# Optimization experiments

Hardware: AMD Instinct MI355X
Metric: run time of the kernel (lower is better)

## Reference

```python
import jax, jax.numpy as jnp
import numpy as np

EMB_DIM = 256
NUM_EMB = 1024
COMMITMENT = 0.25
DECAY = 0.9
EPS = 1e-5
B, H, W = 32, 64, 64


def setup_inputs() -> dict:
    key = jax.random.key(0)
    k1, k2 = jax.random.split(key)
    x = jax.random.normal(k1, (B, EMB_DIM, H, W), dtype=jnp.float32)
    embed = jax.random.normal(k2, (EMB_DIM, NUM_EMB), dtype=jnp.float32)
    cluster_size = jnp.zeros((NUM_EMB,), dtype=jnp.float32)
    ema_embed = embed  # registered as embed.clone() in the torch module
    return {"x": x, "embed": embed, "cluster_size": cluster_size, "ema_embed": ema_embed}


def reference(x, embed, cluster_size, ema_embed):
    # x: [B, C, H, W] -> [B, H, W, C]
    xp = jnp.transpose(x, (0, 2, 3, 1))
    flat = xp.reshape(-1, EMB_DIM)  # [N, D]
    # squared-distance matrix [N, K]
    dist = (jnp.sum(flat * flat, axis=1, keepdims=True)
            - 2.0 * (flat @ embed)
            + jnp.sum(embed * embed, axis=0, keepdims=True))
    embed_idx_flat = jnp.argmin(dist, axis=1)  # [N]
    embed_idx = embed_idx_flat.reshape(xp.shape[:-1])  # [B, H, W]
    quantize = embed.T[embed_idx]  # gather -> [B, H, W, D]

    # training-mode EMA codebook update (buffer updates in torch)
    ref_count = jax.ops.segment_sum(jnp.ones_like(embed_idx_flat, dtype=flat.dtype),
                                    embed_idx_flat, num_segments=NUM_EMB)  # [K]
    new_cluster_size = cluster_size * DECAY + (1.0 - DECAY) * ref_count
    n = jnp.sum(new_cluster_size)
    smoothing = n * ((new_cluster_size + EPS) / (n + new_cluster_size * EPS))
    # dw = flatten^T @ onehot, computed as a segment sum: [K, D] -> [D, K]
    dw = jax.ops.segment_sum(flat, embed_idx_flat, num_segments=NUM_EMB).T
    new_ema_embed = ema_embed * DECAY + (1.0 - DECAY) * dw
    new_embed = new_ema_embed / smoothing[None, :]

    e_latent_loss = jnp.mean((jax.lax.stop_gradient(quantize) - xp) ** 2)
    loss = COMMITMENT * e_latent_loss
    # straight-through estimator
    quantize_st = xp + jax.lax.stop_gradient(quantize - xp)
    out = jnp.transpose(quantize_st, (0, 3, 1, 2))  # [B, C, H, W]
    return out, loss, embed_idx, new_embed, new_cluster_size, new_ema_embed
```

## Files before the change

kernel.cpp:

```cpp
#include <hip/hip_runtime.h>
#include <cfloat>
#include <cstdint>

typedef unsigned short u16;

#define NTOK   131072
#define DIM    256
#define NCODE  1024
#define HW     4096
#define PLANE  1048576
#define DECAYF 0.9f
#define EPSF   1e-5f

#define O_OUT     0
#define O_LOSS    33554432
#define O_IDX     33554433
#define O_NEWEMB  33685505
#define O_NCS     33947649
#define O_NEE     33948673

#define P_XS      0
#define P_V1      16777216
#define P_V2      17825792
#define P_KK      18874368
#define P_VF      19922944
#define P_DW      20054016
#define P_BT      22151168
#define P_ENORM64 22413312

#define WS_ENORM  0
#define WS_CNT    1024
#define WS_LOSS   2048
#define WS_RC     2049
#define WS_LIST   2050
#define WS_SMOOTH 34818

#define REF_CAP 32768
#define DELTA   0.25f
#define RT      16

typedef __attribute__((ext_vector_type(8))) short bf16x8;
typedef __attribute__((ext_vector_type(4))) float f32x4;

__device__ __forceinline__ u16 bf16_rne(float f) {
    unsigned int u = __float_as_uint(f);
    unsigned int r = u + 0x7FFF + ((u >> 16) & 1);
    return (u16)(r >> 16);
}
__device__ __forceinline__ float bf16_to_f(u16 s) {
    return __uint_as_float(((unsigned int)s) << 16);
}
__device__ __forceinline__ void gload_lds16(const void* g, void* l) {
    __builtin_amdgcn_global_load_lds(
        (const __attribute__((address_space(1))) unsigned int*)g,
        (__attribute__((address_space(3))) unsigned int*)l, 16, 0, 0);
}

__global__ void k_enorm(const float* __restrict__ embed, float* __restrict__ enorm,
                        double* __restrict__ enorm64) {
    int k = blockIdx.x * 256 + threadIdx.x;
    double s = 0.0;
    for (int d = 0; d < DIM; ++d) {
        float e = embed[(size_t)d * NCODE + k];
        s += (double)e * (double)e;
    }
    enorm[k] = (float)s;
    enorm64[k] = s;
}

__global__ __launch_bounds__(256) void k_xs(const float* __restrict__ x,
                                            u16* __restrict__ Xs,
                                            float* __restrict__ loss_acc)
{
    __shared__ float tile[64 * 65];
    __shared__ float red[256];
    const int tid = threadIdx.x;
    const int blk = blockIdx.x;
    const int b = blk >> 8;
    const int dc = (blk >> 6) & 3;
    const int hwc = blk & 63;
    const int d0 = dc * 64, hw0 = hwc * 64;
    const int r = tid >> 2, s = tid & 3;
    float sq = 0.f;
#pragma unroll
    for (int j = 0; j < 4; ++j) {
        float4 v = *(const float4*)&x[(size_t)b * PLANE + (size_t)(d0 + r) * HW + hw0 + s * 16 + j * 4];
        int c = s * 16 + j * 4;
        tile[r * 65 + c + 0] = v.x; tile[r * 65 + c + 1] = v.y;
        tile[r * 65 + c + 2] = v.z; tile[r * 65 + c + 3] = v.w;
        sq = fmaf(v.x, v.x, sq); sq = fmaf(v.y, v.y, sq);
        sq = fmaf(v.z, v.z, sq); sq = fmaf(v.w, v.w, sq);
    }
    __syncthreads();
    const int tk = tid >> 2, dq = tid & 3;
    u16 us[16];
#pragma unroll
    for (int j = 0; j < 16; ++j)
        us[j] = bf16_rne(tile[(dq * 16 + j) * 65 + tk]);
    size_t ob = (size_t)(b * 4096 + hw0 + tk) * 256 + d0 + dq * 16;
    *(uint4*)&Xs[ob]     = *(uint4*)&us[0];
    *(uint4*)&Xs[ob + 8] = *(uint4*)&us[8];
    red[tid] = sq; __syncthreads();
    for (int st = 128; st > 0; st >>= 1) {
        if (tid < st) red[tid] += red[tid + st];
        __syncthreads();
    }
    if (tid == 0) atomicAdd(loss_acc, red[0]);
}

__global__ __launch_bounds__(256) void k_bt(const float* __restrict__ embed, u16* __restrict__ Bt)
{
    const int tile = blockIdx.x;
    const int cc = tile >> 4, kc = tile & 15;
    const int seg = kc >> 3, dbase = (kc & 7) * 32;
    const int tid = threadIdx.x;
#pragma unroll
    for (int g2 = 0; g2 < 2; ++g2) {
        int p = g2 * 256 + tid;
        int n = p >> 2, s = p & 3, lg = (s - n) & 3;
        int code = cc * 128 + n;
        u16 us[8];
#pragma unroll
        for (int e = 0; e < 8; ++e) {
            int d = dbase + lg * 8 + e;
            float E = embed[(size_t)d * NCODE + code];
            u16 hi = bf16_rne(E);
            us[e] = seg ? bf16_rne(E - bf16_to_f(hi)) : hi;
        }
        *(uint4*)&Bt[(size_t)tile * 4096 + (size_t)p * 8] = *(uint4*)&us[0];
    }
}

__global__ __launch_bounds__(256) void k_dist(
    const u16* __restrict__ Xs, const u16* __restrict__ Bt,
    const float* __restrict__ enorm,
    float* __restrict__ pv1, float* __restrict__ pv2, float* __restrict__ pkk)
{
    __shared__ __align__(16) u16 lds[12288];
    const int tid = threadIdx.x;
    const int w = tid >> 6, l = tid & 63;
    const int cc = blockIdx.x >> 10;
    const int n0 = (blockIdx.x & 1023) * 128;
    const int mh = w & 1, nh = w >> 1;
    const int lane15 = l & 15, quad = l >> 4;

    const u16* src[6];
    u16* dst[6];
#pragma unroll
    for (int r = 0; r < 6; ++r) {
        int p = r * 256 + w * 64 + l;
        dst[r] = &lds[(size_t)(r * 256 + w * 64) * 8];
        if (p < 512) {
            int m = p >> 2, s = p & 3, lg = (s - m) & 3;
            src[r] = Xs + (size_t)(n0 + m) * 256 + lg * 8;
        } else {
            int q = p - 512;
            int kcb = (q >> 9) * 8;
            int qq = q & 511;
            src[r] = Bt + (size_t)(cc * 16 + kcb) * 4096 + (size_t)qq * 8;
        }
    }

    f32x4 acc[4][4];
#pragma unroll
    for (int i = 0; i < 4; ++i)
#pragma unroll
        for (int j = 0; j < 4; ++j) acc[i][j] = (f32x4)0.f;

    for (int kc8 = 0; kc8 < 8; ++kc8) {
        __syncthreads();
#pragma unroll
        for (int r = 0; r < 6; ++r) {
            const u16* s = src[r] + (r < 2 ? (size_t)kc8 * 32 : (size_t)kc8 * 4096);
            gload_lds16(s, dst[r]);
        }
        __syncthreads();

        bf16x8 af[4];
#pragma unroll
        for (int mt = 0; mt < 4; ++mt) {
            int m = mh * 64 + mt * 16 + lane15;
            int slot = (quad + m) & 3;
            af[mt] = *(const bf16x8*)&lds[(size_t)(m * 4 + slot) * 8];
        }
#pragma unroll
        for (int seg = 0; seg < 2; ++seg) {
#pragma unroll
            for (int nt = 0; nt < 4; ++nt) {
                int n = nh * 64 + nt * 16 + lane15;
                int slot = (quad + n) & 3;
                bf16x8 bfr = *(const bf16x8*)&lds[(size_t)(512 + seg * 512 + n * 4 + slot) * 8];
#pragma unroll
                for (int mt = 0; mt < 4; ++mt)
                    acc[mt][nt] = __builtin_amdgcn_mfma_f32_16x16x32_bf16(af[mt], bfr, acc[mt][nt], 0, 0, 0);
            }
        }
    }

    float ev[4]; int ec[4];
#pragma unroll
    for (int nt = 0; nt < 4; ++nt) {
        ec[nt] = cc * 128 + nh * 64 + nt * 16 + lane15;
        ev[nt] = enorm[ec[nt]];
    }
    float r1[4][4], r2[4][4]; int rk[4][4];
#pragma unroll
    for (int mt = 0; mt < 4; ++mt)
#pragma unroll
        for (int rg = 0; rg < 4; ++rg) {
            float v1 = FLT_MAX, v2 = FLT_MAX; int k1 = 1 << 30;
#pragma unroll
            for (int nt = 0; nt < 4; ++nt) {
                float d = fmaf(-2.f, acc[mt][nt][rg], ev[nt]);
                if (d < v1) { v2 = v1; v1 = d; k1 = ec[nt]; }
                else v2 = fminf(v2, d);
            }
            r1[mt][rg] = v1; r2[mt][rg] = v2; rk[mt][rg] = k1;
        }
#pragma unroll
    for (int mask = 1; mask <= 8; mask <<= 1) {
#pragma unroll
        for (int mt = 0; mt < 4; ++mt)
#pragma unroll
            for (int rg = 0; rg < 4; ++rg) {
                float ov1 = __shfl_xor(r1[mt][rg], mask);
                float ov2 = __shfl_xor(r2[mt][rg], mask);
                int   ok  = __shfl_xor(rk[mt][rg], mask);
                if (ov1 < r1[mt][rg] || (ov1 == r1[mt][rg] && ok < rk[mt][rg])) {
                    r2[mt][rg] = fminf(r1[mt][rg], ov2);
                    r1[mt][rg] = ov1; rk[mt][rg] = ok;
                } else {
                    r2[mt][rg] = fminf(r2[mt][rg], ov1);
                }
            }
    }
    __syncthreads();
    float* epi = (float*)lds;
    if (lane15 == 0) {
#pragma unroll
        for (int mt = 0; mt < 4; ++mt)
#pragma unroll
            for (int rg = 0; rg < 4; ++rg) {
                int t = mh * 64 + mt * 16 + quad * 4 + rg;
                float* p = &epi[(nh * 128 + t) * 3];
                p[0] = r1[mt][rg]; p[1] = r2[mt][rg]; p[2] = __int_as_float(rk[mt][rg]);
            }
    }
    __syncthreads();
    if (tid < 128) {
        const float* p0 = &epi[tid * 3];
        const float* p1 = &epi[(128 + tid) * 3];
        float v1 = p0[0], v2 = p0[1]; int k1 = __float_as_int(p0[2]);
        float a1 = p1[0], a2 = p1[1]; int ak = __float_as_int(p1[2]);
        if (a1 < v1 || (a1 == v1 && ak < k1)) { v2 = fminf(v1, a2); v1 = a1; k1 = ak; }
        else v2 = fminf(v2, a1);
        size_t o = (size_t)cc * NTOK + n0 + tid;
        pv1[o] = v1; pv2[o] = v2; pkk[o] = (float)k1;
    }
}

__global__ __launch_bounds__(256) void k_amin(
    const float* __restrict__ pv1, const float* __restrict__ pv2, const float* __restrict__ pkk,
    float* __restrict__ out_idx, float* __restrict__ vf, float* __restrict__ loss_acc,
    int* __restrict__ refcnt, int* __restrict__ reflist)
{
    const int n = blockIdx.x * 256 + threadIdx.x;
    float v1 = FLT_MAX, v2 = FLT_MAX; int k1 = 1 << 30;
    for (int cc = 0; cc < 8; ++cc) {
        float a1 = pv1[(size_t)cc * NTOK + n], a2 = pv2[(size_t)cc * NTOK + n];
        int ak = (int)pkk[(size_t)cc * NTOK + n];
        if (a1 < v1 || (a1 == v1 && ak < k1)) { v2 = fminf(v1, a2); v1 = a1; k1 = ak; }
        else v2 = fminf(v2, a1);
    }
    out_idx[n] = (float)k1;
    vf[n] = v1;
    if (v2 - v1 < DELTA) {
        int pos = atomicAdd(refcnt, 1);
        if (pos < REF_CAP) reflist[pos] = n;
    }
    __shared__ float red[256];
    red[threadIdx.x] = v1; __syncthreads();
    for (int s = 128; s > 0; s >>= 1) {
        if (threadIdx.x < s) red[threadIdx.x] += red[threadIdx.x + s];
        __syncthreads();
    }
    if (threadIdx.x == 0) atomicAdd(loss_acc, red[0]);
}

__global__ __launch_bounds__(256) void k_refine(
    const float* __restrict__ x, const float* __restrict__ embed,
    const double* __restrict__ enorm64,
    float* __restrict__ out_idx, const int* __restrict__ refcnt,
    const int* __restrict__ reflist, const float* __restrict__ vf,
    float* __restrict__ loss_acc)
{
    __shared__ double xm2[RT][DIM];
    __shared__ int toks[RT];
    __shared__ double wv[4][RT];
    __shared__ int wk[4][RT];
    const int tid = threadIdx.x;
    const int w = tid >> 6, l = tid & 63;
    const int cnt = min(*refcnt, REF_CAP);
    for (int base = blockIdx.x * RT; base < cnt; base += gridDim.x * RT) {
        const int nb = min(RT, cnt - base);
        for (int j = 0; j < nb; ++j) {
            int n = reflist[base + j];
            if (tid == 0) toks[j] = n;
            int b = n >> 12, hw = n & 4095;
            float xv = x[(size_t)b * PLANE + (size_t)tid * HW + hw];
            xm2[j][tid] = -2.0 * (double)xv;
        }
        __syncthreads();

        double bv[RT]; int bk[RT];
#pragma unroll
        for (int j = 0; j < RT; ++j) { bv[j] = 1e300; bk[j] = 0; }
#pragma unroll 1
        for (int c = 0; c < 4; ++c) {
            const int k = c * 256 + tid;
            double acc[RT];
#pragma unroll
            for (int j = 0; j < RT; ++j) acc[j] = 0.0;
            const float* ep = embed + k;
#pragma unroll 4
            for (int d = 0; d < DIM; ++d) {
                double ed = (double)ep[(size_t)d * NCODE];
#pragma unroll
                for (int j = 0; j < RT; ++j)
                    acc[j] = fma(ed, xm2[j][d], acc[j]);
            }
            double e2 = enorm64[k];
#pragma unroll
            for (int j = 0; j < RT; ++j) {
                double dist = e2 + acc[j];
                if (dist < bv[j]) { bv[j] = dist; bk[j] = k; }
            }
        }

#pragma unroll
        for (int j = 0; j < RT; ++j) {
            double v = bv[j]; int kk = bk[j];
#pragma unroll
            for (int m = 1; m < 64; m <<= 1) {
                double ov = __shfl_xor(v, m);
                int ok = __shfl_xor(kk, m);
                if (ov < v || (ov == v && ok < kk)) { v = ov; kk = ok; }
            }
            if (l == 0) { wv[w][j] = v; wk[w][j] = kk; }
        }
        __syncthreads();
        if (tid < nb) {
            double v = wv[0][tid]; int kk = wk[0][tid];
#pragma unroll
            for (int wi = 1; wi < 4; ++wi) {
                double ov = wv[wi][tid]; int ok = wk[wi][tid];
                if (ov < v || (ov == v && ok < kk)) { v = ov; kk = ok; }
            }
            int n = toks[tid];
            out_idx[n] = (float)kk;
            atomicAdd(loss_acc, (float)(v - (double)vf[n]));
        }
        __syncthreads();
    }
}

__global__ __launch_bounds__(256) void k_cnt(const float* __restrict__ out_idx, float* __restrict__ cnt) {
    const int n = blockIdx.x * 256 + threadIdx.x;
    atomicAdd(&cnt[(int)out_idx[n]], 1.0f);
}

__global__ __launch_bounds__(256) void k_dw(
    const float* __restrict__ x, const float* __restrict__ out_idx, float* __restrict__ part)
{
    __shared__ float tile[NCODE * 9];
    const int tid = threadIdx.x;
    const int slice = blockIdx.x & 31;
    const int chunk = blockIdx.x >> 5;
    const int d0 = slice * 8;
    for (int i = tid; i < NCODE * 9; i += 256) tile[i] = 0.f;
    __syncthreads();
    const int nbeg = chunk * (NTOK / 8);
    for (int t = tid; t < NTOK / 8; t += 256) {
        const int n = nbeg + t;
        const int b = n >> 12, hw = n & 4095;
        const int k = (int)out_idx[n];
        const float* xb = x + (size_t)b * PLANE + hw;
        float* tp = tile + k * 9;
#pragma unroll
        for (int dl = 0; dl < 8; ++dl)
            unsafeAtomicAdd(&tp[dl], xb[(size_t)(d0 + dl) * HW]);
    }
    __syncthreads();
    for (int i = tid; i < 8 * NCODE; i += 256) {
        const int dl = i >> 10, k = i & (NCODE - 1);
        part[((size_t)chunk * DIM + d0 + dl) * NCODE + k] = tile[k * 9 + dl];
    }
}

__global__ __launch_bounds__(1024) void k_fin_cs(
    const float* __restrict__ cs_in, const float* __restrict__ cnt,
    float* __restrict__ out_ncs, float* __restrict__ smooth)
{
    const int k = threadIdx.x;
    float ncs = cs_in[k] * DECAYF + (1.f - DECAYF) * cnt[k];
    out_ncs[k] = ncs;
    __shared__ float red[1024];
    red[k] = ncs; __syncthreads();
    for (int s = 512; s > 0; s >>= 1) {
        if (k < s) red[k] += red[k + s];
        __syncthreads();
    }
    float n = red[0];
    smooth[k] = n * ((ncs + EPSF) / (n + ncs * EPSF));
}

__global__ __launch_bounds__(256) void k_fin_emb(
    const float* __restrict__ ema, const float* __restrict__ part,
    const float* __restrict__ smooth, float* __restrict__ out_ne, float* __restrict__ out_nee)
{
    const int i = blockIdx.x * 256 + threadIdx.x;
    const int k = i & (NCODE - 1);
    float dw = 0.f;
    for (int c = 0; c < 8; ++c) dw += part[(size_t)c * (DIM * NCODE) + i];
    float nee = ema[i] * DECAYF + (1.f - DECAYF) * dw;
    out_nee[i] = nee;
    out_ne[i] = nee / smooth[k];
}

__global__ __launch_bounds__(256) void k_quant(
    const float* __restrict__ embed, const float* __restrict__ out_idx, float* __restrict__ out_q)
{
    const int n = blockIdx.x * 256 + threadIdx.x;
    const int b = n >> 12, hw = n & 4095;
    const int idx = (int)out_idx[n];
    const size_t base = (size_t)b * PLANE + hw;
    for (int d = 0; d < DIM; ++d)
        out_q[base + (size_t)d * HW] = embed[(size_t)d * NCODE + idx];
}

__global__ void k_loss(const float* __restrict__ loss_acc, float* __restrict__ out_loss) {
    out_loss[0] = 0.25f * loss_acc[0] / 33554432.f;
}

extern "C" void kernel_launch(void* const* d_in, const int* in_sizes, int n_in,
                              void* d_out, int out_size, void* d_ws, size_t ws_size,
                              hipStream_t stream) {
    const float* x     = (const float*)d_in[0];
    const float* embed = (const float*)d_in[1];
    const float* csz   = (const float*)d_in[2];
    const float* ema   = (const float*)d_in[3];
    float* out = (float*)d_out;
    float* ws  = (float*)d_ws;

    u16* Xs = (u16*)(out + P_XS);
    u16* Bt = (u16*)(out + P_BT);
    double* enorm64 = (double*)(out + P_ENORM64);

    hipMemsetAsync(ws + WS_CNT, 0, (size_t)(WS_RC + 1 - WS_CNT) * sizeof(float), stream);

    k_enorm<<<4, 256, 0, stream>>>(embed, ws + WS_ENORM, enorm64);
    k_xs<<<8192, 256, 0, stream>>>(x, Xs, ws + WS_LOSS);
    k_bt<<<128, 256, 0, stream>>>(embed, Bt);
    k_dist<<<8192, 256, 0, stream>>>(Xs, Bt, ws + WS_ENORM,
                                     out + P_V1, out + P_V2, out + P_KK);
    k_amin<<<NTOK / 256, 256, 0, stream>>>(out + P_V1, out + P_V2, out + P_KK,
                                           out + O_IDX, out + P_VF, ws + WS_LOSS,
                                           (int*)(ws + WS_RC), (int*)(ws + WS_LIST));
    k_refine<<<1024, 256, 0, stream>>>(x, embed, enorm64, out + O_IDX,
                                       (const int*)(ws + WS_RC), (const int*)(ws + WS_LIST),
                                       out + P_VF, ws + WS_LOSS);
    k_cnt<<<NTOK / 256, 256, 0, stream>>>(out + O_IDX, ws + WS_CNT);
    k_dw<<<256, 256, 0, stream>>>(x, out + O_IDX, out + P_DW);
    k_fin_cs<<<1, 1024, 0, stream>>>(csz, ws + WS_CNT, out + O_NCS, ws + WS_SMOOTH);
    k_fin_emb<<<1024, 256, 0, stream>>>(ema, out + P_DW, ws + WS_SMOOTH,
                                        out + O_NEWEMB, out + O_NEE);
    k_quant<<<NTOK / 256, 256, 0, stream>>>(embed, out + O_IDX, out + O_OUT);
    k_loss<<<1, 1, 0, stream>>>(ws + WS_LOSS, out + O_LOSS);
}
```

Measured before the change: 1.215 ms.

## Fuse argmin into distance GEMM with resident X tile and triple-buffered codebook

Each distance block now owns 128 tokens and loops over all 8 code chunks. The full X tile stays resident in LDS, and codebook slices stream through a 3-deep ring with explicit vmcnt waits. The running top-2 reduction is done in registers, which removes the partial-result buffers and the separate k_amin kernel. The LDS swizzle also changes (an extra m>>2 term) to reduce bank conflicts. In exchange it uses about 119KB of LDS per block, which limits occupancy to one block per CU, and the grid drops to 1024 blocks.

```diff
diff --git a/kernel.cpp b/kernel.cpp
--- a/kernel.cpp
+++ b/kernel.cpp
@@ -20,9 +20,6 @@
 #define O_NEE     33948673
 
 #define P_XS      0
-#define P_V1      16777216
-#define P_V2      17825792
-#define P_KK      18874368
 #define P_VF      19922944
 #define P_DW      20054016
 #define P_BT      22151168
@@ -117,7 +114,7 @@
 #pragma unroll
     for (int g2 = 0; g2 < 2; ++g2) {
         int p = g2 * 256 + tid;
-        int n = p >> 2, s = p & 3, lg = (s - n) & 3;
+        int n = p >> 2, s = p & 3, lg = (s - n - (n >> 2)) & 3;
         int code = cc * 128 + n;
         u16 us[8];
 #pragma unroll
@@ -134,157 +131,166 @@
 __global__ __launch_bounds__(256) void k_dist(
     const u16* __restrict__ Xs, const u16* __restrict__ Bt,
     const float* __restrict__ enorm,
-    float* __restrict__ pv1, float* __restrict__ pv2, float* __restrict__ pkk)
-{
-    __shared__ __align__(16) u16 lds[12288];
+    float* __restrict__ out_idx, float* __restrict__ vfo, float* __restrict__ loss_acc,
+    int* __restrict__ refcnt, int* __restrict__ reflist)
+{
+    __shared__ __align__(16) u16 lds[60928];
     const int tid = threadIdx.x;
     const int w = tid >> 6, l = tid & 63;
-    const int cc = blockIdx.x >> 10;
-    const int n0 = (blockIdx.x & 1023) * 128;
+    const int n0 = blockIdx.x * 128;
     const int mh = w & 1, nh = w >> 1;
     const int lane15 = l & 15, quad = l >> 4;
 
-    const u16* src[6];
-    u16* dst[6];
-#pragma unroll
-    for (int r = 0; r < 6; ++r) {
-        int p = r * 256 + w * 64 + l;
-        dst[r] = &lds[(size_t)(r * 256 + w * 64) * 8];
-        if (p < 512) {
-            int m = p >> 2, s = p & 3, lg = (s - m) & 3;
-            src[r] = Xs + (size_t)(n0 + m) * 256 + lg * 8;
-        } else {
-            int q = p - 512;
-            int kcb = (q >> 9) * 8;
-            int qq = q & 511;
-            src[r] = Bt + (size_t)(cc * 16 + kcb) * 4096 + (size_t)qq * 8;
-        }
-    }
-
-    f32x4 acc[4][4];
-#pragma unroll
-    for (int i = 0; i < 4; ++i)
-#pragma unroll
-        for (int j = 0; j < 4; ++j) acc[i][j] = (f32x4)0.f;
-
-    for (int kc8 = 0; kc8 < 8; ++kc8) {
-        __syncthreads();
-#pragma unroll
-        for (int r = 0; r < 6; ++r) {
-            const u16* s = src[r] + (r < 2 ? (size_t)kc8 * 32 : (size_t)kc8 * 4096);
-            gload_lds16(s, dst[r]);
-        }
-        __syncthreads();
-
-        bf16x8 af[4];
-#pragma unroll
-        for (int mt = 0; mt < 4; ++mt) {
-            int m = mh * 64 + mt * 16 + lane15;
-            int slot = (quad + m) & 3;
-            af[mt] = *(const bf16x8*)&lds[(size_t)(m * 4 + slot) * 8];
-        }
-#pragma unroll
-        for (int seg = 0; seg < 2; ++seg) {
-#pragma unroll
-            for (int nt = 0; nt < 4; ++nt) {
-                int n = nh * 64 + nt * 16 + lane15;
-                int slot = (quad + n) & 3;
-                bf16x8 bfr = *(const bf16x8*)&lds[(size_t)(512 + seg * 512 + n * 4 + slot) * 8];
-#pragma unroll
-                for (int mt = 0; mt < 4; ++mt)
-                    acc[mt][nt] = __builtin_amdgcn_mfma_f32_16x16x32_bf16(af[mt], bfr, acc[mt][nt], 0, 0, 0);
-            }
-        }
-    }
-
-    float ev[4]; int ec[4];
-#pragma unroll
-    for (int nt = 0; nt < 4; ++nt) {
-        ec[nt] = cc * 128 + nh * 64 + nt * 16 + lane15;
-        ev[nt] = enorm[ec[nt]];
-    }
-    float r1[4][4], r2[4][4]; int rk[4][4];
-#pragma unroll
-    for (int mt = 0; mt < 4; ++mt)
-#pragma unroll
-        for (int rg = 0; rg < 4; ++rg) {
-            float v1 = FLT_MAX, v2 = FLT_MAX; int k1 = 1 << 30;
-#pragma unroll
-            for (int nt = 0; nt < 4; ++nt) {
-                float d = fmaf(-2.f, acc[mt][nt][rg], ev[nt]);
-                if (d < v1) { v2 = v1; v1 = d; k1 = ec[nt]; }
-                else v2 = fminf(v2, d);
-            }
-            r1[mt][rg] = v1; r2[mt][rg] = v2; rk[mt][rg] = k1;
-        }
-#pragma unroll
-    for (int mask = 1; mask <= 8; mask <<= 1) {
+#pragma unroll
+    for (int rr = 0; rr < 16; ++rr) {
+        int p = rr * 256 + tid;
+        int kc8p = p >> 9;
+        int q = p & 511;
+        int m = q >> 2, s = q & 3;
+        int lg = (s - m - (m >> 2)) & 3;
+        gload_lds16(Xs + (size_t)(n0 + m) * 256 + kc8p * 32 + lg * 8,
+                    &lds[(size_t)(rr * 256 + w * 64) * 8]);
+    }
+    gload_lds16((const char*)enorm + (size_t)tid * 16,
+                &lds[58880 + (size_t)(w * 64) * 8]);
+
+#define STAGE_B(cc_, kc8_, ring_) do {                                               \
+    _Pragma("unroll")                                                                \
+    for (int rr_ = 0; rr_ < 4; ++rr_) {                                              \
+        int p_ = rr_ * 256 + tid;                                                    \
+        int seg_ = p_ >> 9;                                                          \
+        gload_lds16(Bt + (size_t)((cc_) * 16 + seg_ * 8 + (kc8_)) * 4096             \
+                       + (size_t)(p_ & 511) * 8,                                     \
+                    &lds[32768 + (ring_) * 8192 + (size_t)(rr_ * 256 + w * 64) * 8]); \
+    } } while (0)
+
+    STAGE_B(0, 0, 0);
+    STAGE_B(0, 1, 1);
+
+    float rv1 = FLT_MAX, rv2 = FLT_MAX; int rk1 = 1 << 30;
+    float* epi = (float*)&lds[57344];
+    const float* enf = (const float*)&lds[58880];
+
+    for (int cc = 0; cc < 8; ++cc) {
+        f32x4 acc[4][4];
+#pragma unroll
+        for (int i = 0; i < 4; ++i)
+#pragma unroll
+            for (int j = 0; j < 4; ++j) acc[i][j] = (f32x4)0.f;
+
+#pragma unroll
+        for (int kc8 = 0; kc8 < 8; ++kc8) {
+            const int i = cc * 8 + kc8;
+            if (cc == 7 && kc8 == 7) asm volatile("s_waitcnt vmcnt(0)" ::: "memory");
+            else                     asm volatile("s_waitcnt vmcnt(4)" ::: "memory");
+            __builtin_amdgcn_s_barrier();
+
+            if (i + 2 < 64) {
+                const int i2 = i + 2;
+                STAGE_B(i2 >> 3, i2 & 7, i2 % 3);
+            }
+
+            const u16* bufB = &lds[32768 + (i % 3) * 8192];
+            bf16x8 af[4];
+#pragma unroll
+            for (int mt = 0; mt < 4; ++mt) {
+                int m = mh * 64 + mt * 16 + lane15;
+                int slot = (quad + m + (m >> 2)) & 3;
+                af[mt] = *(const bf16x8*)&lds[(size_t)kc8 * 4096 + (size_t)(m * 4 + slot) * 8];
+            }
+#pragma unroll
+            for (int seg = 0; seg < 2; ++seg)
+#pragma unroll
+                for (int nt = 0; nt < 4; ++nt) {
+                    int n = nh * 64 + nt * 16 + lane15;
+                    int slot = (quad + n + (n >> 2)) & 3;
+                    bf16x8 bfr = *(const bf16x8*)&bufB[(size_t)(seg * 512 + n * 4 + slot) * 8];
+#pragma unroll
+                    for (int mt = 0; mt < 4; ++mt)
+                        acc[mt][nt] = __builtin_amdgcn_mfma_f32_16x16x32_bf16(af[mt], bfr, acc[mt][nt], 0, 0, 0);
+                }
+        }
+
+        float ev[4]; int ec[4];
+#pragma unroll
+        for (int nt = 0; nt < 4; ++nt) {
+            ec[nt] = cc * 128 + nh * 64 + nt * 16 + lane15;
+            ev[nt] = enf[ec[nt]];
+        }
+        float r1[4][4], r2[4][4]; int rk[4][4];
 #pragma unroll
         for (int mt = 0; mt < 4; ++mt)
 #pragma unroll
             for (int rg = 0; rg < 4; ++rg) {
-                float ov1 = __shfl_xor(r1[mt][rg], mask);
-                float ov2 = __shfl_xor(r2[mt][rg], mask);
-                int   ok  = __shfl_xor(rk[mt][rg], mask);
-                if (ov1 < r1[mt][rg] || (ov1 == r1[mt][rg] && ok < rk[mt][rg])) {
-                    r2[mt][rg] = fminf(r1[mt][rg], ov2);
-                    r1[mt][rg] = ov1; rk[mt][rg] = ok;
-                } else {
-                    r2[mt][rg] = fminf(r2[mt][rg], ov1);
+                float v1 = FLT_MAX, v2 = FLT_MAX; int k1 = 1 << 30;
+#pragma unroll
+                for (int nt = 0; nt < 4; ++nt) {
+                    float d = fmaf(-2.f, acc[mt][nt][rg], ev[nt]);
+                    if (d < v1) { v2 = v1; v1 = d; k1 = ec[nt]; }
+                    else v2 = fminf(v2, d);
                 }
-            }
+                r1[mt][rg] = v1; r2[mt][rg] = v2; rk[mt][rg] = k1;
+            }
+#pragma unroll
+        for (int mask = 1; mask <= 8; mask <<= 1) {
+#pragma unroll
+            for (int mt = 0; mt < 4; ++mt)
+#pragma unroll
+                for (int rg = 0; rg < 4; ++rg) {
+                    float ov1 = __shfl_xor(r1[mt][rg], mask);
+                    float ov2 = __shfl_xor(r2[mt][rg], mask);
+                    int   ok  = __shfl_xor(rk[mt][rg], mask);
+                    if (ov1 < r1[mt][rg] || (ov1 == r1[mt][rg] && ok < rk[mt][rg])) {
+                        r2[mt][rg] = fminf(r1[mt][rg], ov2);
+                        r1[mt][rg] = ov1; rk[mt][rg] = ok;
+                    } else {
+                        r2[mt][rg] = fminf(r2[mt][rg], ov1);
+                    }
+                }
+        }
+        if (lane15 == 0) {
+#pragma unroll
+            for (int mt = 0; mt < 4; ++mt)
+#pragma unroll
+                for (int rg = 0; rg < 4; ++rg) {
+                    int t = mh * 64 + mt * 16 + quad * 4 + rg;
+                    float* p = &epi[(nh * 128 + t) * 3];
+                    p[0] = r1[mt][rg]; p[1] = r2[mt][rg]; p[2] = __int_as_float(rk[mt][rg]);
+                }
+        }
+        asm volatile("s_waitcnt lgkmcnt(0)" ::: "memory");
+        __builtin_amdgcn_s_barrier();
+        if (tid < 128) {
+            const float* p0 = &epi[tid * 3];
+            const float* p1 = &epi[(128 + tid) * 3];
+            float v1 = p0[0], v2 = p0[1]; int k1 = __float_as_int(p0[2]);
+            float a1 = p1[0], a2 = p1[1]; int ak = __float_as_int(p1[2]);
+            if (a1 < v1 || (a1 == v1 && ak < k1)) { v2 = fminf(v1, a2); v1 = a1; k1 = ak; }
+            else v2 = fminf(v2, a1);
+            if (v1 < rv1 || (v1 == rv1 && k1 < rk1)) { rv2 = fminf(rv1, v2); rv1 = v1; rk1 = k1; }
+            else rv2 = fminf(rv2, v1);
+        }
+    }
+
+    if (tid < 128) {
+        int n = n0 + tid;
+        out_idx[n] = (float)rk1;
+        vfo[n] = rv1;
+        if (rv2 - rv1 < DELTA) {
+            int pos = atomicAdd(refcnt, 1);
+            if (pos < REF_CAP) reflist[pos] = n;
+        }
     }
     __syncthreads();
-    float* epi = (float*)lds;
-    if (lane15 == 0) {
-#pragma unroll
-        for (int mt = 0; mt < 4; ++mt)
-#pragma unroll
-            for (int rg = 0; rg < 4; ++rg) {
-                int t = mh * 64 + mt * 16 + quad * 4 + rg;
-                float* p = &epi[(nh * 128 + t) * 3];
-                p[0] = r1[mt][rg]; p[1] = r2[mt][rg]; p[2] = __int_as_float(rk[mt][rg]);
-            }
-    }
+    float* red = epi;
+    red[tid] = (tid < 128) ? rv1 : 0.f;
     __syncthreads();
-    if (tid < 128) {
-        const float* p0 = &epi[tid * 3];
-        const float* p1 = &epi[(128 + tid) * 3];
-        float v1 = p0[0], v2 = p0[1]; int k1 = __float_as_int(p0[2]);
-        float a1 = p1[0], a2 = p1[1]; int ak = __float_as_int(p1[2]);
-        if (a1 < v1 || (a1 == v1 && ak < k1)) { v2 = fminf(v1, a2); v1 = a1; k1 = ak; }
-        else v2 = fminf(v2, a1);
-        size_t o = (size_t)cc * NTOK + n0 + tid;
-        pv1[o] = v1; pv2[o] = v2; pkk[o] = (float)k1;
-    }
-}
-
-__global__ __launch_bounds__(256) void k_amin(
-    const float* __restrict__ pv1, const float* __restrict__ pv2, const float* __restrict__ pkk,
-    float* __restrict__ out_idx, float* __restrict__ vf, float* __restrict__ loss_acc,
-    int* __restrict__ refcnt, int* __restrict__ reflist)
-{
-    const int n = blockIdx.x * 256 + threadIdx.x;
-    float v1 = FLT_MAX, v2 = FLT_MAX; int k1 = 1 << 30;
-    for (int cc = 0; cc < 8; ++cc) {
-        float a1 = pv1[(size_t)cc * NTOK + n], a2 = pv2[(size_t)cc * NTOK + n];
-        int ak = (int)pkk[(size_t)cc * NTOK + n];
-        if (a1 < v1 || (a1 == v1 && ak < k1)) { v2 = fminf(v1, a2); v1 = a1; k1 = ak; }
-        else v2 = fminf(v2, a1);
-    }
-    out_idx[n] = (float)k1;
-    vf[n] = v1;
-    if (v2 - v1 < DELTA) {
-        int pos = atomicAdd(refcnt, 1);
-        if (pos < REF_CAP) reflist[pos] = n;
-    }
-    __shared__ float red[256];
-    red[threadIdx.x] = v1; __syncthreads();
     for (int s = 128; s > 0; s >>= 1) {
-        if (threadIdx.x < s) red[threadIdx.x] += red[threadIdx.x + s];
-        __syncthreads();
-    }
-    if (threadIdx.x == 0) atomicAdd(loss_acc, red[0]);
+        if (tid < s) red[tid] += red[tid + s];
+        __syncthreads();
+    }
+    if (tid == 0) atomicAdd(loss_acc, red[0]);
+#undef STAGE_B
 }
 
 __global__ __launch_bounds__(256) void k_refine(
@@ -461,11 +467,9 @@
     k_enorm<<<4, 256, 0, stream>>>(embed, ws + WS_ENORM, enorm64);
     k_xs<<<8192, 256, 0, stream>>>(x, Xs, ws + WS_LOSS);
     k_bt<<<128, 256, 0, stream>>>(embed, Bt);
-    k_dist<<<8192, 256, 0, stream>>>(Xs, Bt, ws + WS_ENORM,
-                                     out + P_V1, out + P_V2, out + P_KK);
-    k_amin<<<NTOK / 256, 256, 0, stream>>>(out + P_V1, out + P_V2, out + P_KK,
-                                           out + O_IDX, out + P_VF, ws + WS_LOSS,
-                                           (int*)(ws + WS_RC), (int*)(ws + WS_LIST));
+    k_dist<<<1024, 256, 0, stream>>>(Xs, Bt, ws + WS_ENORM,
+                                     out + O_IDX, out + P_VF, ws + WS_LOSS,
+                                     (int*)(ws + WS_RC), (int*)(ws + WS_LIST));
     k_refine<<<1024, 256, 0, stream>>>(x, embed, enorm64, out + O_IDX,
                                        (const int*)(ws + WS_RC), (const int*)(ws + WS_LIST),
                                        out + P_VF, ws + WS_LOSS);
```

After: 1.303 ms. 1.07x slower.

## Add fp32 refinement pass before fp64 refine, routing only near-ties to double

Applied to the files above, without the earlier changes.

Inserts an fp32 re-scoring kernel for tokens flagged by the bf16 distance pass. Tokens whose top-2 fp32 gap exceeds a margin are finalised there. Only the remaining near-ties go to a hard list that the existing fp64 refine kernel processes. This cuts the expensive double-precision work on MI355X, at the risk that the fp32 margin occasionally picks a different argmin than fp64 would.

```diff
diff --git a/kernel.cpp b/kernel.cpp
--- a/kernel.cpp
+++ b/kernel.cpp
@@ -27,16 +27,19 @@
 #define P_DW      20054016
 #define P_BT      22151168
 #define P_ENORM64 22413312
+#define P_HLIST   22415360
 
 #define WS_ENORM  0
 #define WS_CNT    1024
 #define WS_LOSS   2048
 #define WS_RC     2049
-#define WS_LIST   2050
-#define WS_SMOOTH 34818
+#define WS_RC2    2050
+#define WS_LIST   2051
+#define WS_SMOOTH 34819
 
 #define REF_CAP 32768
 #define DELTA   0.25f
+#define MARGIN  0.03f
 #define RT      16
 
 typedef __attribute__((ext_vector_type(8))) short bf16x8;
@@ -287,11 +290,107 @@
     if (threadIdx.x == 0) atomicAdd(loss_acc, red[0]);
 }
 
-__global__ __launch_bounds__(256) void k_refine(
+__global__ __launch_bounds__(256) void k_ref32(
+    const float* __restrict__ x, const float* __restrict__ embed,
+    const float* __restrict__ enorm,
+    float* __restrict__ out_idx, const int* __restrict__ refcnt,
+    const int* __restrict__ reflist, const float* __restrict__ vf,
+    float* __restrict__ loss_acc, int* __restrict__ hardcnt, int* __restrict__ hardlist)
+{
+    __shared__ float xm2t[DIM][RT + 1];
+    __shared__ int toks[RT];
+    __shared__ float wv1[4][RT], wv2[4][RT];
+    __shared__ int wk1[4][RT];
+    const int tid = threadIdx.x;
+    const int w = tid >> 6;
+    const int cnt = min(*refcnt, REF_CAP);
+    for (int base = blockIdx.x * RT; base < cnt; base += gridDim.x * RT) {
+        const int nb = min(RT, cnt - base);
+        for (int j = 0; j < nb; ++j) {
+            int n = reflist[base + j];
+            if (tid == 0) toks[j] = n;
+            int b = n >> 12, hw = n & 4095;
+            xm2t[tid][j] = -2.f * x[(size_t)b * PLANE + (size_t)tid * HW + hw];
+        }
+        if (nb < RT)
+            for (int j = nb; j < RT; ++j) xm2t[tid][j] = 0.f;
+        __syncthreads();
+
+        float b1[RT], b2[RT]; int k1[RT];
+#pragma unroll
+        for (int j = 0; j < RT; ++j) { b1[j] = FLT_MAX; b2[j] = FLT_MAX; k1[j] = 1 << 30; }
+#pragma unroll 1
+        for (int c = 0; c < 4; ++c) {
+            const int k = c * 256 + tid;
+            float acc[RT];
+#pragma unroll
+            for (int j = 0; j < RT; ++j) acc[j] = 0.f;
+#pragma unroll 1
+            for (int d0 = 0; d0 < DIM; d0 += 8) {
+                float er[8];
+#pragma unroll
+                for (int dd = 0; dd < 8; ++dd)
+                    er[dd] = embed[(size_t)(d0 + dd) * NCODE + k];
+#pragma unroll
+                for (int dd = 0; dd < 8; ++dd)
+#pragma unroll
+                    for (int j = 0; j < RT; ++j)
+                        acc[j] = fmaf(er[dd], xm2t[d0 + dd][j], acc[j]);
+            }
+            float e2 = enorm[k];
+#pragma unroll
+            for (int j = 0; j < RT; ++j) {
+                float dist = e2 + acc[j];
+                if (dist < b1[j]) { b2[j] = b1[j]; b1[j] = dist; k1[j] = k; }
+                else b2[j] = fminf(b2[j], dist);
+            }
+        }
+
+#pragma unroll
+        for (int m = 1; m < 64; m <<= 1) {
+#pragma unroll
+            for (int j = 0; j < RT; ++j) {
+                float ov1 = __shfl_xor(b1[j], m);
+                float ov2 = __shfl_xor(b2[j], m);
+                int   ok  = __shfl_xor(k1[j], m);
+                if (ov1 < b1[j] || (ov1 == b1[j] && ok < k1[j])) {
+                    b2[j] = fminf(b1[j], ov2); b1[j] = ov1; k1[j] = ok;
+                } else {
+                    b2[j] = fminf(b2[j], ov1);
+                }
+            }
+        }
+        if ((tid & 63) == 0) {
+#pragma unroll
+            for (int j = 0; j < RT; ++j) { wv1[w][j] = b1[j]; wk1[w][j] = k1[j]; wv2[w][j] = b2[j]; }
+        }
+        __syncthreads();
+        if (tid < nb) {
+            float v1 = wv1[0][tid], v2 = wv2[0][tid]; int kk = wk1[0][tid];
+#pragma unroll
+            for (int wi = 1; wi < 4; ++wi) {
+                float a1 = wv1[wi][tid], a2 = wv2[wi][tid]; int ak = wk1[wi][tid];
+                if (a1 < v1 || (a1 == v1 && ak < kk)) { v2 = fminf(v1, a2); v1 = a1; kk = ak; }
+                else v2 = fminf(v2, a1);
+            }
+            int n = toks[tid];
+            if (v2 - v1 > MARGIN) {
+                out_idx[n] = (float)kk;
+                atomicAdd(loss_acc, v1 - vf[n]);
+            } else {
+                int pos = atomicAdd(hardcnt, 1);
+                hardlist[pos] = n;
+            }
+        }
+        __syncthreads();
+    }
+}
+
+__global__ __launch_bounds__(256) void k_ref64(
     const float* __restrict__ x, const float* __restrict__ embed,
     const double* __restrict__ enorm64,
-    float* __restrict__ out_idx, const int* __restrict__ refcnt,
-    const int* __restrict__ reflist, const float* __restrict__ vf,
+    float* __restrict__ out_idx, const int* __restrict__ hcnt,
+    const int* __restrict__ hlist, const float* __restrict__ vf,
     float* __restrict__ loss_acc)
 {
     __shared__ double xm2[RT][DIM];
@@ -300,11 +399,11 @@
     __shared__ int wk[4][RT];
     const int tid = threadIdx.x;
     const int w = tid >> 6, l = tid & 63;
-    const int cnt = min(*refcnt, REF_CAP);
+    const int cnt = min(*hcnt, REF_CAP);
     for (int base = blockIdx.x * RT; base < cnt; base += gridDim.x * RT) {
         const int nb = min(RT, cnt - base);
         for (int j = 0; j < nb; ++j) {
-            int n = reflist[base + j];
+            int n = hlist[base + j];
             if (tid == 0) toks[j] = n;
             int b = n >> 12, hw = n & 4095;
             float xv = x[(size_t)b * PLANE + (size_t)tid * HW + hw];
@@ -456,7 +555,7 @@
     u16* Bt = (u16*)(out + P_BT);
     double* enorm64 = (double*)(out + P_ENORM64);
 
-    hipMemsetAsync(ws + WS_CNT, 0, (size_t)(WS_RC + 1 - WS_CNT) * sizeof(float), stream);
+    hipMemsetAsync(ws + WS_CNT, 0, (size_t)(WS_RC2 + 1 - WS_CNT) * sizeof(float), stream);
 
     k_enorm<<<4, 256, 0, stream>>>(embed, ws + WS_ENORM, enorm64);
     k_xs<<<8192, 256, 0, stream>>>(x, Xs, ws + WS_LOSS);
@@ -466,9 +565,13 @@
     k_amin<<<NTOK / 256, 256, 0, stream>>>(out + P_V1, out + P_V2, out + P_KK,
                                            out + O_IDX, out + P_VF, ws + WS_LOSS,
                                            (int*)(ws + WS_RC), (int*)(ws + WS_LIST));
-    k_refine<<<1024, 256, 0, stream>>>(x, embed, enorm64, out + O_IDX,
-                                       (const int*)(ws + WS_RC), (const int*)(ws + WS_LIST),
-                                       out + P_VF, ws + WS_LOSS);
+    k_ref32<<<2048, 256, 0, stream>>>(x, embed, ws + WS_ENORM, out + O_IDX,
+                                      (const int*)(ws + WS_RC), (const int*)(ws + WS_LIST),
+                                      out + P_VF, ws + WS_LOSS,
+                                      (int*)(ws + WS_RC2), (int*)(out + P_HLIST));
+    k_ref64<<<512, 256, 0, stream>>>(x, embed, enorm64, out + O_IDX,
+                                     (const int*)(ws + WS_RC2), (const int*)(out + P_HLIST),
+                                     out + P_VF, ws + WS_LOSS);
     k_cnt<<<NTOK / 256, 256, 0, stream>>>(out + O_IDX, ws + WS_CNT);
     k_dw<<<256, 256, 0, stream>>>(x, out + O_IDX, out + P_DW);
     k_fin_cs<<<1, 1024, 0, stream>>>(csz, ws + WS_CNT, out + O_NCS, ws + WS_SMOOTH);
```

After: 1.272 ms. 4.7% more time.
